# Optimization experiments

Hardware: AMD Instinct MI355X
Metric: run time of the kernel (lower is better)

The kernel has to match this reference:

```python
import jax, jax.numpy as jnp
import numpy as np

N_NODES = 50000
N_EDGES = 800000
F_IN = 128
HEADS = 4
C_OUT = 32
HID = HEADS * C_OUT  # 128
NEG_SLOPE = 0.2


def _gatv2_layer(x, src, dst, W_l, b_l, W_r, b_r, att, bias, concat):
    """PyG-style GATv2Conv (eval mode, no dropout).
    x: [N, F]; W_*: [F, H*C]; att: [H, C]; bias: [H*C] (concat) or [C] (mean).
    """
    N = x.shape[0]
    H, C = att.shape
    x_l = (x @ W_l + b_l).reshape(N, H, C)  # source transform
    x_r = (x @ W_r + b_r).reshape(N, H, C)  # target transform
    e = jax.nn.leaky_relu(x_l[src] + x_r[dst], NEG_SLOPE)      # [E, H, C]
    logits = jnp.einsum('ehc,hc->eh', e, att)                   # [E, H]
    # segment softmax over incoming edges of each destination node
    m = jax.ops.segment_max(logits, dst, num_segments=N)        # [N, H]
    alpha = jnp.exp(logits - m[dst])
    denom = jax.ops.segment_sum(alpha, dst, num_segments=N)     # [N, H]
    alpha = alpha / (denom[dst] + 1e-16)
    out = jax.ops.segment_sum(x_l[src] * alpha[..., None], dst, num_segments=N)  # [N, H, C]
    out = out.reshape(N, H * C) if concat else out.mean(axis=1)
    return out + bias


def setup_inputs() -> dict:
    key = jax.random.key(0)
    ks = jax.random.split(key, 20)
    s = 0.1
    inp = {
        'x': jax.random.normal(ks[0], (N_NODES, F_IN), dtype=jnp.float32),
        'edge_index': jax.random.randint(ks[1], (2, N_EDGES), 0, N_NODES, dtype=jnp.int64),
        # layer 1: 128 -> 4 heads x 32
        'W_l1': jax.random.normal(ks[2], (F_IN, HID), dtype=jnp.float32) * s,
        'b_l1': jnp.zeros((HID,), dtype=jnp.float32),
        'W_r1': jax.random.normal(ks[3], (F_IN, HID), dtype=jnp.float32) * s,
        'b_r1': jnp.zeros((HID,), dtype=jnp.float32),
        'att1': jax.random.normal(ks[4], (HEADS, C_OUT), dtype=jnp.float32) * s,
        'bias1': jnp.zeros((HID,), dtype=jnp.float32),
        # layer 2: 128 -> 4 heads x 32
        'W_l2': jax.random.normal(ks[5], (HID, HID), dtype=jnp.float32) * s,
        'b_l2': jnp.zeros((HID,), dtype=jnp.float32),
        'W_r2': jax.random.normal(ks[6], (HID, HID), dtype=jnp.float32) * s,
        'b_r2': jnp.zeros((HID,), dtype=jnp.float32),
        'att2': jax.random.normal(ks[7], (HEADS, C_OUT), dtype=jnp.float32) * s,
        'bias2': jnp.zeros((HID,), dtype=jnp.float32),
        # final layer: 128 -> 1 head x 1, concat=False
        'W_l3': jax.random.normal(ks[8], (HID, 1), dtype=jnp.float32) * s,
        'b_l3': jnp.zeros((1,), dtype=jnp.float32),
        'W_r3': jax.random.normal(ks[9], (HID, 1), dtype=jnp.float32) * s,
        'b_r3': jnp.zeros((1,), dtype=jnp.float32),
        'att3': jax.random.normal(ks[10], (1, 1), dtype=jnp.float32) * s,
        'bias3': jnp.zeros((1,), dtype=jnp.float32),
    }
    return inp


def reference(x, edge_index, W_l1, b_l1, W_r1, b_r1, att1, bias1,
              W_l2, b_l2, W_r2, b_r2, att2, bias2,
              W_l3, b_l3, W_r3, b_r3, att3, bias3):
    src, dst = edge_index[0], edge_index[1]
    h = jax.nn.elu(_gatv2_layer(x, src, dst, W_l1, b_l1, W_r1, b_r1, att1, bias1, True))
    h = jax.nn.elu(_gatv2_layer(h, src, dst, W_l2, b_l2, W_r2, b_r2, att2, bias2, True))
    o = _gatv2_layer(h, src, dst, W_l3, b_l3, W_r3, b_r3, att3, bias3, False)
    return jax.nn.sigmoid(o).reshape(x.shape[0], 1)
```

## Files before the change

kernel.cpp:

```cpp
#include <hip/hip_runtime.h>
#include <hip/hip_bf16.h>
#include <math.h>

#define NN 50000
#define NE 800000

typedef __attribute__((ext_vector_type(8))) short bf16x8;
typedef __attribute__((ext_vector_type(4))) float f32x4;

__device__ __forceinline__ float lrelu(float x) { return x > 0.f ? x : 0.2f * x; }

__device__ __forceinline__ ushort f2bf(float v) {
  __hip_bfloat16 h = __float2bfloat16(v);
  return *(ushort*)&h;
}
__device__ __forceinline__ float bf2f(ushort u) {
  return __uint_as_float(((unsigned int)u) << 16);
}

__global__ void cvt_bf16(const float* __restrict__ in, ushort* __restrict__ out, int n8) {
  int i = blockIdx.x * 256 + threadIdx.x;
  if (i >= n8) return;
  float4 v0 = *(const float4*)&in[i * 8];
  float4 v1 = *(const float4*)&in[i * 8 + 4];
  ushort4 a, b;
  a.x = f2bf(v0.x); a.y = f2bf(v0.y); a.z = f2bf(v0.z); a.w = f2bf(v0.w);
  b.x = f2bf(v1.x); b.y = f2bf(v1.y); b.z = f2bf(v1.z); b.w = f2bf(v1.w);
  *(ushort4*)&out[i * 8] = a;
  *(ushort4*)&out[i * 8 + 4] = b;
}

__global__ void pack_w(const float* __restrict__ Wl, const float* __restrict__ Wr,
                       ushort* __restrict__ Bpack) {
  int t = blockIdx.x * 256 + threadIdx.x;
  if (t >= 4096) return;
  int hi = t & 3;
  int col = (t >> 2) & 255;
  int kt = t >> 10;
  const float* W = (col < 128) ? (Wl + col) : (Wr + (col - 128));
  ushort4 u0, u1;
  int k0 = kt * 32 + hi * 8;
  u0.x = f2bf(W[(k0 + 0) * 128]); u0.y = f2bf(W[(k0 + 1) * 128]);
  u0.z = f2bf(W[(k0 + 2) * 128]); u0.w = f2bf(W[(k0 + 3) * 128]);
  u1.x = f2bf(W[(k0 + 4) * 128]); u1.y = f2bf(W[(k0 + 5) * 128]);
  u1.z = f2bf(W[(k0 + 6) * 128]); u1.w = f2bf(W[(k0 + 7) * 128]);
  *(ushort4*)&Bpack[t * 8] = u0;
  *(ushort4*)&Bpack[t * 8 + 4] = u1;
}

__global__ __launch_bounds__(256) void gemm_mfma(
    const ushort* __restrict__ Abf, const ushort* __restrict__ Bpack,
    const float* __restrict__ bl, const float* __restrict__ br,
    ushort* __restrict__ Xl, ushort* __restrict__ Xr, int n) {
  const int tid = threadIdx.x;
  const int wv = tid >> 6;
  const int l = tid & 63;
  const int lr = l & 15;
  const int hi = l >> 4;
  const int r0 = blockIdx.x * 64;

  f32x4 acc[4][4];
#pragma unroll
  for (int mi = 0; mi < 4; ++mi)
#pragma unroll
    for (int nj = 0; nj < 4; ++nj) acc[mi][nj] = (f32x4)0.f;

#pragma unroll
  for (int kt = 0; kt < 4; ++kt) {
    bf16x8 b[4], a[4];
#pragma unroll
    for (int nj = 0; nj < 4; ++nj) {
      int col = wv * 64 + nj * 16 + lr;
      b[nj] = *(const bf16x8*)&Bpack[((kt * 256 + col) * 4 + hi) * 8];
    }
#pragma unroll
    for (int mi = 0; mi < 4; ++mi) {
      int row = r0 + mi * 16 + lr;
      row = row < n ? row : n - 1;
      a[mi] = *(const bf16x8*)&Abf[row * 128 + kt * 32 + hi * 8];
    }
#pragma unroll
    for (int mi = 0; mi < 4; ++mi)
#pragma unroll
      for (int nj = 0; nj < 4; ++nj)
        acc[mi][nj] = __builtin_amdgcn_mfma_f32_16x16x32_bf16(a[mi], b[nj], acc[mi][nj], 0, 0, 0);
  }

#pragma unroll
  for (int nj = 0; nj < 4; ++nj) {
    int col = wv * 64 + nj * 16 + lr;
    float bb = (col < 128) ? bl[col] : br[col - 128];
    ushort* dst = (col < 128) ? (Xl + col) : (Xr + (col - 128));
#pragma unroll
    for (int mi = 0; mi < 4; ++mi) {
#pragma unroll
      for (int v = 0; v < 4; ++v) {
        int row = r0 + mi * 16 + hi * 4 + v;
        if (row < n) dst[row * 128] = f2bf(acc[mi][nj][v] + bb);
      }
    }
  }
}

__global__ void zero_i32(int* p, int n) {
  int i = blockIdx.x * 256 + threadIdx.x;
  if (i < n) p[i] = 0;
}

__global__ void hist_kernel(const int* __restrict__ dst, int* __restrict__ deg) {
  int e = blockIdx.x * 256 + threadIdx.x;
  if (e < NE) atomicAdd(&deg[dst[e]], 1);
}

__global__ __launch_bounds__(256) void scan_a(const int* __restrict__ in,
                                              int* __restrict__ excl,
                                              int* __restrict__ bsum, int n) {
  int i = blockIdx.x * 256 + threadIdx.x;
  int v = (i < n) ? in[i] : 0;
  int lane = threadIdx.x & 63, wid = threadIdx.x >> 6;
  int incl = v;
#pragma unroll
  for (int off = 1; off < 64; off <<= 1) {
    int u = __shfl_up(incl, off);
    if (lane >= off) incl += u;
  }
  __shared__ int wsum[4];
  if (lane == 63) wsum[wid] = incl;
  __syncthreads();
  int wo = 0;
  for (int w = 0; w < wid; w++) wo += wsum[w];
  if (i < n) excl[i] = wo + incl - v;
  if (threadIdx.x == 255 && bsum) bsum[blockIdx.x] = wo + incl;
}

__global__ void scan_c(int* __restrict__ rowptr, const int* __restrict__ boff,
                       int* __restrict__ cursor, int n) {
  int i = blockIdx.x * 256 + threadIdx.x;
  if (i < n) {
    int v = rowptr[i] + boff[i >> 8];
    rowptr[i] = v;
    cursor[i] = v;
  } else if (i == n) {
    rowptr[n] = NE;
  }
}

__global__ void scatter_kernel(const int* __restrict__ src, const int* __restrict__ dst,
                               int* __restrict__ cursor, int* __restrict__ ssort) {
  int e = blockIdx.x * 256 + threadIdx.x;
  if (e >= NE) return;
  int p = atomicAdd(&cursor[dst[e]], 1);
  ssort[p] = src[e];
}

template <int MODE>
__global__ __launch_bounds__(256) void gat_aggregate(
    const ushort* __restrict__ Xl, const ushort* __restrict__ Xr,
    const float* __restrict__ att, const int* __restrict__ ssort,
    const int* __restrict__ rowptr, const float* __restrict__ bias,
    ushort* __restrict__ outb,
    const float* __restrict__ Wl3, const float* __restrict__ Wr3,
    const float* __restrict__ bl3, const float* __restrict__ br3,
    float* __restrict__ xl3, float* __restrict__ xr3) {
  int slot = threadIdx.x >> 5;
  int l = threadIdx.x & 31;
  int n = blockIdx.x * 8 + slot;
  if (n >= NN) return;
  int s0 = rowptr[n], s1 = rowptr[n + 1];
  ushort4 xru = *(const ushort4*)&Xr[n * 128 + l * 4];
  float4 xr = make_float4(bf2f(xru.x), bf2f(xru.y), bf2f(xru.z), bf2f(xru.w));
  float4 at = *(const float4*)&att[l * 4];

  float den0 = 0.f, den1 = 0.f;
  float4 A0 = make_float4(0.f, 0.f, 0.f, 0.f);
  float4 A1 = make_float4(0.f, 0.f, 0.f, 0.f);

  int i = s0;
  for (; i + 4 <= s1; i += 4) {
    int sa = ssort[i], sb = ssort[i + 1], sc = ssort[i + 2], sd = ssort[i + 3];
    ushort4 ua = *(const ushort4*)&Xl[sa * 128 + l * 4];
    ushort4 ub = *(const ushort4*)&Xl[sb * 128 + l * 4];
    ushort4 uc = *(const ushort4*)&Xl[sc * 128 + l * 4];
    ushort4 ud = *(const ushort4*)&Xl[sd * 128 + l * 4];
    float4 xa = make_float4(bf2f(ua.x), bf2f(ua.y), bf2f(ua.z), bf2f(ua.w));
    float4 xb = make_float4(bf2f(ub.x), bf2f(ub.y), bf2f(ub.z), bf2f(ub.w));
    float4 xc = make_float4(bf2f(uc.x), bf2f(uc.y), bf2f(uc.z), bf2f(uc.w));
    float4 xd = make_float4(bf2f(ud.x), bf2f(ud.y), bf2f(ud.z), bf2f(ud.w));
    float pa = at.x * lrelu(xa.x + xr.x) + at.y * lrelu(xa.y + xr.y) +
               at.z * lrelu(xa.z + xr.z) + at.w * lrelu(xa.w + xr.w);
    float pb = at.x * lrelu(xb.x + xr.x) + at.y * lrelu(xb.y + xr.y) +
               at.z * lrelu(xb.z + xr.z) + at.w * lrelu(xb.w + xr.w);
    float pc = at.x * lrelu(xc.x + xr.x) + at.y * lrelu(xc.y + xr.y) +
               at.z * lrelu(xc.z + xr.z) + at.w * lrelu(xc.w + xr.w);
    float pd = at.x * lrelu(xd.x + xr.x) + at.y * lrelu(xd.y + xr.y) +
               at.z * lrelu(xd.z + xr.z) + at.w * lrelu(xd.w + xr.w);
#pragma unroll
    for (int off = 1; off <= 4; off <<= 1) {
      pa += __shfl_xor(pa, off);
      pb += __shfl_xor(pb, off);
      pc += __shfl_xor(pc, off);
      pd += __shfl_xor(pd, off);
    }
    float wa = __expf(fminf(pa, 30.f));
    float wb = __expf(fminf(pb, 30.f));
    float wc = __expf(fminf(pc, 30.f));
    float wd = __expf(fminf(pd, 30.f));
    den0 += wa + wc;
    den1 += wb + wd;
    A0.x += wa * xa.x + wc * xc.x;  A1.x += wb * xb.x + wd * xd.x;
    A0.y += wa * xa.y + wc * xc.y;  A1.y += wb * xb.y + wd * xd.y;
    A0.z += wa * xa.z + wc * xc.z;  A1.z += wb * xb.z + wd * xd.z;
    A0.w += wa * xa.w + wc * xc.w;  A1.w += wb * xb.w + wd * xd.w;
  }
  for (; i < s1; ++i) {
    int sa = ssort[i];
    ushort4 ua = *(const ushort4*)&Xl[sa * 128 + l * 4];
    float4 xa = make_float4(bf2f(ua.x), bf2f(ua.y), bf2f(ua.z), bf2f(ua.w));
    float pa = at.x * lrelu(xa.x + xr.x) + at.y * lrelu(xa.y + xr.y) +
               at.z * lrelu(xa.z + xr.z) + at.w * lrelu(xa.w + xr.w);
#pragma unroll
    for (int off = 1; off <= 4; off <<= 1) pa += __shfl_xor(pa, off);
    float wa = __expf(fminf(pa, 30.f));
    den0 += wa;
    A0.x += wa * xa.x; A0.y += wa * xa.y; A0.z += wa * xa.z; A0.w += wa * xa.w;
  }
  float den = den0 + den1;
  float inv = 1.f / (den + 1e-16f);
  float4 b4 = *(const float4*)&bias[l * 4];
  float4 o;
  o.x = (A0.x + A1.x) * inv + b4.x;
  o.y = (A0.y + A1.y) * inv + b4.y;
  o.z = (A0.z + A1.z) * inv + b4.z;
  o.w = (A0.w + A1.w) * inv + b4.w;
  o.x = o.x > 0.f ? o.x : __expf(o.x) - 1.f;
  o.y = o.y > 0.f ? o.y : __expf(o.y) - 1.f;
  o.z = o.z > 0.f ? o.z : __expf(o.z) - 1.f;
  o.w = o.w > 0.f ? o.w : __expf(o.w) - 1.f;
  if (MODE == 0) {
    ushort4 ub;
    ub.x = f2bf(o.x); ub.y = f2bf(o.y); ub.z = f2bf(o.z); ub.w = f2bf(o.w);
    *(ushort4*)&outb[n * 128 + l * 4] = ub;
  } else {
    float4 wl = *(const float4*)&Wl3[l * 4];
    float4 wr = *(const float4*)&Wr3[l * 4];
    float sl = o.x * wl.x + o.y * wl.y + o.z * wl.z + o.w * wl.w;
    float sr = o.x * wr.x + o.y * wr.y + o.z * wr.z + o.w * wr.w;
#pragma unroll
    for (int off = 1; off <= 16; off <<= 1) {
      sl += __shfl_xor(sl, off);
      sr += __shfl_xor(sr, off);
    }
    if (l == 0) {
      xl3[n] = sl + bl3[0];
      xr3[n] = sr + br3[0];
    }
  }
}

__global__ __launch_bounds__(256) void aggregate3_fused(
    const float* __restrict__ xl3, const float* __restrict__ xr3,
    const float* __restrict__ att, const int* __restrict__ ssort,
    const int* __restrict__ rowptr, const float* __restrict__ bias,
    float* __restrict__ out, int nn) {
  int wid = threadIdx.x >> 6, lane = threadIdx.x & 63;
  int n = blockIdx.x * 4 + wid;
  if (n >= nn) return;
  int s0 = rowptr[n], s1 = rowptr[n + 1];
  float xr = xr3[n];
  float a0 = att[0];
  float den = 0.f, acc = 0.f;
  for (int i = s0 + lane; i < s1; i += 64) {
    float xl = xl3[ssort[i]];
    float v = xl + xr;
    float p = a0 * (v > 0.f ? v : 0.2f * v);
    float w = __expf(fminf(p, 30.f));
    den += w;
    acc += w * xl;
  }
#pragma unroll
  for (int off = 32; off; off >>= 1) {
    den += __shfl_xor(den, off);
    acc += __shfl_xor(acc, off);
  }
  if (lane == 0) {
    float o = acc / (den + 1e-16f) + bias[0];
    out[n] = 1.f / (1.f + __expf(-o));
  }
}

extern "C" void kernel_launch(void* const* d_in, const int* in_sizes, int n_in,
                              void* d_out, int out_size, void* d_ws, size_t ws_size,
                              hipStream_t stream) {
  const float* x = (const float*)d_in[0];
  const int* ei = (const int*)d_in[1];
  const int* src = ei;
  const int* dst = ei + NE;
  const float* W_l1 = (const float*)d_in[2];
  const float* b_l1 = (const float*)d_in[3];
  const float* W_r1 = (const float*)d_in[4];
  const float* b_r1 = (const float*)d_in[5];
  const float* att1 = (const float*)d_in[6];
  const float* bias1 = (const float*)d_in[7];
  const float* W_l2 = (const float*)d_in[8];
  const float* b_l2 = (const float*)d_in[9];
  const float* W_r2 = (const float*)d_in[10];
  const float* b_r2 = (const float*)d_in[11];
  const float* att2 = (const float*)d_in[12];
  const float* bias2 = (const float*)d_in[13];
  const float* W_l3 = (const float*)d_in[14];
  const float* b_l3 = (const float*)d_in[15];
  const float* W_r3 = (const float*)d_in[16];
  const float* b_r3 = (const float*)d_in[17];
  const float* att3 = (const float*)d_in[18];
  const float* bias3 = (const float*)d_in[19];
  float* out = (float*)d_out;

  ushort* xbb = (ushort*)d_ws;
  ushort* xl_b = xbb + NN * 128;
  ushort* xr_b = xl_b + NN * 128;
  ushort* bpack = xr_b + NN * 128;
  int* deg = (int*)(bpack + 32768);
  int* rowptr = deg + NN;
  int* cursor = rowptr + NN + 1;
  int* bsum = cursor + NN;
  int* boff = bsum + 256;
  int* ssort = boff + 256;
  float* xl3 = (float*)(ssort + NE);
  float* xr3 = xl3 + NN;

  const int NB_N = (NN + 255) / 256;
  const int NB_E = (NE + 255) / 256;
  const int NB_G = (NN + 63) / 64;
  const int NB_A = (NN + 7) / 8;
  const int NB_W4 = (NN + 3) / 4;
  const int NB_C = (NN * 128 / 8 + 255) / 256;

  zero_i32<<<NB_N, 256, 0, stream>>>(deg, NN);
  hist_kernel<<<NB_E, 256, 0, stream>>>(dst, deg);
  scan_a<<<NB_N, 256, 0, stream>>>(deg, rowptr, bsum, NN);
  scan_a<<<1, 256, 0, stream>>>(bsum, boff, (int*)nullptr, NB_N);
  scan_c<<<NB_N + 1, 256, 0, stream>>>(rowptr, boff, cursor, NN);
  scatter_kernel<<<NB_E, 256, 0, stream>>>(src, dst, cursor, ssort);

  cvt_bf16<<<NB_C, 256, 0, stream>>>(x, xbb, NN * 128 / 8);
  pack_w<<<16, 256, 0, stream>>>(W_l1, W_r1, bpack);
  gemm_mfma<<<NB_G, 256, 0, stream>>>(xbb, bpack, b_l1, b_r1, xl_b, xr_b, NN);
  gat_aggregate<0><<<NB_A, 256, 0, stream>>>(xl_b, xr_b, att1, ssort, rowptr, bias1,
                                             xbb, nullptr, nullptr, nullptr, nullptr,
                                             nullptr, nullptr);

  pack_w<<<16, 256, 0, stream>>>(W_l2, W_r2, bpack);
  gemm_mfma<<<NB_G, 256, 0, stream>>>(xbb, bpack, b_l2, b_r2, xl_b, xr_b, NN);
  gat_aggregate<1><<<NB_A, 256, 0, stream>>>(xl_b, xr_b, att2, ssort, rowptr, bias2,
                                             nullptr, W_l3, W_r3, b_l3, b_r3,
                                             xl3, xr3);

  aggregate3_fused<<<NB_W4, 256, 0, stream>>>(xl3, xr3, att3, ssort, rowptr, bias3, out, NN);
}
```

Measured before the change: 368.9 us.

## Replace per-edge global atomic CSR scatter with two-pass bucketed counting sort

The CSR build no longer does one global atomic per edge on a per-node cursor. Edges are first binned into buckets of 128 destination nodes, using shared-memory counts and one global atomic per bucket per block, and written as (src,dst) pairs. A second kernel then places each pair into its final slot with shared-memory atomics. This removes contended, scattered global atomics and random writes, at the cost of an extra kernel launch and an extra pass that writes and reads the pair array.

```diff
diff --git a/kernel.cpp b/kernel.cpp
--- a/kernel.cpp
+++ b/kernel.cpp
@@ -4,6 +4,8 @@
 
 #define NN 50000
 #define NE 800000
+#define NBUK 391
+#define BNODES 128
 
 typedef __attribute__((ext_vector_type(8))) short bf16x8;
 typedef __attribute__((ext_vector_type(4))) float f32x4;
@@ -134,23 +136,67 @@
 }
 
 __global__ void scan_c(int* __restrict__ rowptr, const int* __restrict__ boff,
-                       int* __restrict__ cursor, int n) {
+                       int* __restrict__ bcur, int n) {
   int i = blockIdx.x * 256 + threadIdx.x;
   if (i < n) {
     int v = rowptr[i] + boff[i >> 8];
     rowptr[i] = v;
-    cursor[i] = v;
+    if ((i & 127) == 0) bcur[i >> 7] = v;
   } else if (i == n) {
     rowptr[n] = NE;
   }
 }
 
-__global__ void scatter_kernel(const int* __restrict__ src, const int* __restrict__ dst,
-                               int* __restrict__ cursor, int* __restrict__ ssort) {
-  int e = blockIdx.x * 256 + threadIdx.x;
-  if (e >= NE) return;
-  int p = atomicAdd(&cursor[dst[e]], 1);
-  ssort[p] = src[e];
+__global__ __launch_bounds__(256) void bucket_scatter(
+    const int* __restrict__ src, const int* __restrict__ dst,
+    int* __restrict__ bcur, int2* __restrict__ pairs) {
+  __shared__ int cnt[NBUK];
+  __shared__ int base[NBUK];
+  const int t = threadIdx.x;
+  for (int i = t; i < NBUK; i += 256) cnt[i] = 0;
+  __syncthreads();
+  const int e0 = blockIdx.x * 4096;
+#pragma unroll
+  for (int j = 0; j < 16; ++j) {
+    int e = e0 + j * 256 + t;
+    if (e < NE) atomicAdd(&cnt[dst[e] >> 7], 1);
+  }
+  __syncthreads();
+  for (int i = t; i < NBUK; i += 256) {
+    int c = cnt[i];
+    base[i] = c ? atomicAdd(&bcur[i], c) : 0;
+    cnt[i] = 0;
+  }
+  __syncthreads();
+#pragma unroll
+  for (int j = 0; j < 16; ++j) {
+    int e = e0 + j * 256 + t;
+    if (e < NE) {
+      int d = dst[e];
+      int b = d >> 7;
+      int r = atomicAdd(&cnt[b], 1);
+      pairs[base[b] + r] = make_int2(src[e], d);
+    }
+  }
+}
+
+__global__ __launch_bounds__(256) void bucket_sort(
+    const int2* __restrict__ pairs, const int* __restrict__ rowptr,
+    int* __restrict__ ssort) {
+  __shared__ int cur[BNODES];
+  const int b = blockIdx.x;
+  const int n0 = b * BNODES;
+  const int t = threadIdx.x;
+  const int n1 = min(n0 + BNODES, NN);
+  if (t < BNODES && n0 + t < NN) cur[t] = rowptr[n0 + t];
+  __syncthreads();
+  const int e0 = rowptr[n0];
+  const int e1 = rowptr[n1];
+  for (int e = e0 + t; e < e1; e += 256) {
+    int2 p = pairs[e];
+    int pos = atomicAdd(&cur[p.y - n0], 1);
+    ssort[pos] = p.x;
+  }
 }
 
 template <int MODE>
@@ -321,11 +367,12 @@
   ushort* bpack = xr_b + NN * 128;
   int* deg = (int*)(bpack + 32768);
   int* rowptr = deg + NN;
-  int* cursor = rowptr + NN + 1;
-  int* bsum = cursor + NN;
+  int* bcur = rowptr + NN + 1;
+  int* bsum = bcur + NBUK;
   int* boff = bsum + 256;
   int* ssort = boff + 256;
-  float* xl3 = (float*)(ssort + NE);
+  int2* pairs = (int2*)(ssort + NE);
+  float* xl3 = (float*)(pairs + NE);
   float* xr3 = xl3 + NN;
 
   const int NB_N = (NN + 255) / 256;
@@ -334,13 +381,15 @@
   const int NB_A = (NN + 7) / 8;
   const int NB_W4 = (NN + 3) / 4;
   const int NB_C = (NN * 128 / 8 + 255) / 256;
+  const int NB_BK = (NE + 4095) / 4096;
 
   zero_i32<<<NB_N, 256, 0, stream>>>(deg, NN);
   hist_kernel<<<NB_E, 256, 0, stream>>>(dst, deg);
   scan_a<<<NB_N, 256, 0, stream>>>(deg, rowptr, bsum, NN);
   scan_a<<<1, 256, 0, stream>>>(bsum, boff, (int*)nullptr, NB_N);
-  scan_c<<<NB_N + 1, 256, 0, stream>>>(rowptr, boff, cursor, NN);
-  scatter_kernel<<<NB_E, 256, 0, stream>>>(src, dst, cursor, ssort);
+  scan_c<<<NB_N + 1, 256, 0, stream>>>(rowptr, boff, bcur, NN);
+  bucket_scatter<<<NB_BK, 256, 0, stream>>>(src, dst, bcur, pairs);
+  bucket_sort<<<NBUK, 256, 0, stream>>>(pairs, rowptr, ssort);
 
   cvt_bf16<<<NB_C, 256, 0, stream>>>(x, xbb, NN * 128 / 8);
   pack_w<<<16, 256, 0, stream>>>(W_l1, W_r1, bpack);
```

Result: faster. 343.9 us (-6.8%).
